# Performance work log

Measured on AMD Instinct MI355X. Metric: run time of the kernel, lower is better.

The kernel has to match this reference:

```python
import jax, jax.numpy as jnp
import numpy as np

H = 1024
B_SZ = 4
L = 2048


def setup_inputs() -> dict:
    key = jax.random.key(0)
    ks = jax.random.split(key, 7)
    s_in = 1.0 / np.sqrt(H)
    x = jax.random.normal(ks[0], (B_SZ, L, H), dtype=jnp.float32)
    # torch nn.Linear weights: (out_features, in_features)
    W_proj = jax.random.uniform(ks[1], (4 * H, H), minval=-s_in, maxval=s_in, dtype=jnp.float32)
    W_delta = jax.random.uniform(ks[2], (H, H), minval=-s_in, maxval=s_in, dtype=jnp.float32)
    b_delta = jax.random.uniform(ks[3], (H,), minval=-s_in, maxval=s_in, dtype=jnp.float32)
    A = 0.02 * jax.random.normal(ks[4], (1, 1, H), dtype=jnp.float32)
    Bp = 0.02 * jax.random.normal(ks[5], (1, H, 1), dtype=jnp.float32)
    D = jnp.ones((1,), dtype=jnp.float32)
    return {"x": x, "W_proj": W_proj, "A": A, "Bp": Bp, "D": D, "W_delta": W_delta, "b_delta": b_delta}


def reference(x, W_proj, A, Bp, D, W_delta, b_delta):
    # x: (b, l, h)
    h = x.shape[-1]
    proj = x @ W_proj.T                                   # (b, l, 4h)
    delta, Bs, Cs, residual = jnp.split(proj, 4, axis=-1) # each (b, l, h)
    delta = jax.nn.softplus(delta @ W_delta.T + b_delta)  # (b, l, h)
    A1 = A[0, 0]       # (h,)
    B1 = Bp[0, :, 0]   # (h,)
    # discretization: dA[b,h,l] = exp(delta*A)[b,l,h] * B1[h] (n-dim of Bp has size 1)
    dA = jnp.exp(delta * A1) * B1                         # (b, l, h), layout transposed vs torch
    # dB[b,h,0,l] = cumsum_l(delta[b,l,h] * B1[h])
    dB = jnp.cumsum(delta * B1, axis=1)                   # (b, l, h)
    # selective_scan: y[b,h,l] = sum_n (dA[b,h,l]*u[b,h,n] + dB[b,h,0,l]) * C[b,h,n]
    # sum over n distributes: y = dA * sum_n(u*C) + dB * sum_n(C)
    uC = jnp.sum(x * Cs, axis=1, keepdims=True)           # (b, 1, h)
    Csum = jnp.sum(Cs, axis=1, keepdims=True)             # (b, 1, h)
    y = dA * uC + dB * Csum                               # (b, l, h)
    return y + residual * D
```

## Files before the change

### kernel.cpp

```cpp
#include <hip/hip_runtime.h>
#include <hip/hip_bf16.h>
#include <cstdint>

#define H 1024
#define BSZ 4
#define LSEQ 2048
#define M_TOT (BSZ*LSEQ)
#define NCH 32
#define LCH (LSEQ/NCH)

typedef __attribute__((ext_vector_type(4))) float  f32x4;
typedef __attribute__((ext_vector_type(2))) float  f32x2;
typedef __attribute__((ext_vector_type(8))) __bf16 bf16x8;
typedef __attribute__((ext_vector_type(4))) __bf16 bf16x4;
typedef __attribute__((ext_vector_type(2))) __bf16 bf16x2;

typedef __attribute__((address_space(1))) unsigned int as1_u32;
typedef __attribute__((address_space(3))) unsigned int as3_u32;

__device__ __forceinline__ void gld_lds16(const void* g, const void* l) {
    as1_u32* gp = reinterpret_cast<as1_u32*>((uintptr_t)g);
    as3_u32* lp = reinterpret_cast<as3_u32*>((uint32_t)(uintptr_t)l);
    __builtin_amdgcn_global_load_lds(gp, lp, 16, 0, 0);
}

__device__ __forceinline__ float softplus_fast(float f) {
    return fmaxf(f, 0.f) + __logf(1.f + __expf(-fabsf(f)));
}

template<int KT, int MODE>
__global__ __launch_bounds__(256, 3) void gemm_bt(
    const __bf16* __restrict__ A,
    const __bf16* __restrict__ B,
    __bf16* __restrict__ O0,
    __bf16* __restrict__ O2,
    const __bf16* __restrict__ xb,
    const float* __restrict__ bias,
    float* __restrict__ pD,
    float* __restrict__ pUp,
    float* __restrict__ pCp)
{
    constexpr int K = KT * 32;
    __shared__ __align__(16) __bf16 lds[17408];

    const int tid  = threadIdx.x;
    const int lane = tid & 63;
    const int wid  = tid >> 6;
    const int wr   = (wid >> 1) * 64;
    const int wc   = (wid & 1) * 64;
    const int l15  = lane & 15;
    const int quad = lane >> 4;

    const int row0 = blockIdx.y * 128;
    const int col0 = blockIdx.x * 128;

    const int srow = lane >> 2;
    const int soct = (lane & 3) ^ ((lane >> 3) & 3);
    const __bf16* ag0 = A + (size_t)(row0 + (wid    )*16 + srow) * K + soct*8;
    const __bf16* ag1 = A + (size_t)(row0 + (wid + 4)*16 + srow) * K + soct*8;
    const __bf16* bg0 = B + (size_t)(col0 + (wid    )*16 + srow) * K + soct*8;
    const __bf16* bg1 = B + (size_t)(col0 + (wid + 4)*16 + srow) * K + soct*8;
    const int lA0 = (wid    )*512;
    const int lA1 = (wid + 4)*512;
    const int lB0 = 4096 + (wid    )*512;
    const int lB1 = 4096 + (wid + 4)*512;

    const int sw = (l15 >> 1) & 3;
    int aoff[4], boff[4];
#pragma unroll
    for (int i = 0; i < 4; ++i) {
        aoff[i] =        ((wr + i*16 + l15) * 4 + (quad ^ sw)) * 8;
        boff[i] = 4096 + ((wc + i*16 + l15) * 4 + (quad ^ sw)) * 8;
    }

    f32x4 acc[4][4] = {};

    auto stage = [&](int buf) {
        __bf16* base = lds + buf * 8192;
        gld_lds16(ag0, base + lA0);
        gld_lds16(ag1, base + lA1);
        gld_lds16(bg0, base + lB0);
        gld_lds16(bg1, base + lB1);
        ag0 += 32; ag1 += 32; bg0 += 32; bg1 += 32;
    };
    auto compute = [&](int buf) {
        const __bf16* base = lds + buf * 8192;
        bf16x8 af[4], bf[4];
#pragma unroll
        for (int i = 0; i < 4; ++i) af[i] = *(const bf16x8*)(base + aoff[i]);
#pragma unroll
        for (int j = 0; j < 4; ++j) bf[j] = *(const bf16x8*)(base + boff[j]);
#pragma unroll
        for (int i = 0; i < 4; ++i)
#pragma unroll
            for (int j = 0; j < 4; ++j)
                acc[i][j] = __builtin_amdgcn_mfma_f32_16x16x32_bf16(
                    af[i], bf[j], acc[i][j], 0, 0, 0);
    };

    stage(0);
#pragma unroll 2
    for (int kt = 0; kt < KT; ++kt) {
        __syncthreads();
        if (kt + 1 < KT) stage((kt + 1) & 1);
        compute(kt & 1);
    }

    const int colb = (col0 & 1023) + wc + l15;
    const int rowb = row0 + wr + quad*4;

    if (MODE == 0) {
#pragma unroll
        for (int i = 0; i < 4; ++i)
#pragma unroll
            for (int j = 0; j < 4; ++j) {
                const int col = colb + j*16;
#pragma unroll
                for (int r = 0; r < 4; ++r)
                    O0[(size_t)(rowb + i*16 + r) * H + col] = (__bf16)acc[i][j][r];
            }
    } else {
        const int seg = col0 >> 10;
        if (seg == 0) {
            const int chunk = (row0 + wr) >> 6;
#pragma unroll
            for (int j = 0; j < 4; ++j) {
                const int col = colb + j*16;
                const float bv = bias[col];
                float s = 0.f;
#pragma unroll
                for (int i = 0; i < 4; ++i)
#pragma unroll
                    for (int r = 0; r < 4; ++r) {
                        float f = softplus_fast(acc[i][j][r] + bv);
                        O0[(size_t)(rowb + i*16 + r) * H + col] = (__bf16)f;
                        s += f;
                    }
                s += __shfl_down(s, 32); s += __shfl_down(s, 16);
                if (quad == 0) pD[chunk*H + col] = s;
            }
        } else if (seg == 1) {
            __syncthreads();
#pragma unroll
            for (int i = 0; i < 4; ++i)
#pragma unroll
                for (int j = 0; j < 4; ++j) {
                    const int lrow0 = wr + quad*4 + i*16;
                    const int lcol  = wc + j*16 + l15;
#pragma unroll
                    for (int r = 0; r < 4; ++r)
                        lds[(lrow0 + r)*136 + lcol] = (__bf16)acc[i][j][r];
                }
            __syncthreads();
            const int g   = tid >> 4;
            const int oct = tid & 15;
            const int gc0 = (col0 & 1023) + oct*8;
            float su[8] = {}, sc[8] = {};
#pragma unroll
            for (int rr = 0; rr < 8; ++rr) {
                const int lrow = g*8 + rr;
                bf16x8 cv = *(const bf16x8*)(lds + lrow*136 + oct*8);
                bf16x8 xv = *(const bf16x8*)(xb + (size_t)(row0 + lrow)*H + gc0);
#pragma unroll
                for (int q = 0; q < 8; ++q) {
                    float c = (float)cv[q];
                    su[q] += (float)xv[q] * c;
                    sc[q] += c;
                }
            }
            float* pf = reinterpret_cast<float*>(lds);
            __syncthreads();
#pragma unroll
            for (int q = 0; q < 8; ++q) {
                pf[g*128 + oct*8 + q]        = su[q];
                pf[2048 + g*128 + oct*8 + q] = sc[q];
            }
            __syncthreads();
            const int col = tid & 127;
            const int rb  = row0 >> 7;
            float s = 0.f;
            if (tid < 128) {
#pragma unroll
                for (int g2 = 0; g2 < 16; ++g2) s += pf[g2*128 + col];
                pUp[rb*H + (col0 & 1023) + col] = s;
            } else {
#pragma unroll
                for (int g2 = 0; g2 < 16; ++g2) s += pf[2048 + g2*128 + col];
                pCp[rb*H + (col0 & 1023) + col] = s;
            }
        } else {
#pragma unroll
            for (int i = 0; i < 4; ++i)
#pragma unroll
                for (int j = 0; j < 4; ++j) {
                    const int col = colb + j*16;
#pragma unroll
                    for (int r = 0; r < 4; ++r)
                        O2[(size_t)(rowb + i*16 + r) * H + col] = (__bf16)acc[i][j][r];
                }
        }
    }
}

#define XB 8192
#define PB 2048
#define DB 1024
#define TB 256
__global__ void cast_kernel(const float* __restrict__ x,
                            const float* __restrict__ Wp,
                            const float* __restrict__ Wd,
                            __bf16* __restrict__ xb,
                            __bf16* __restrict__ Wpb,
                            __bf16* __restrict__ Wdb,
                            __bf16* __restrict__ Wp1T)
{
    __shared__ __bf16 tlds[64*65];
    const int t = threadIdx.x;
    const int bidx = blockIdx.x;

    if (bidx < XB + PB + DB) {
        const f32x4* src; __bf16* dst; int si, di;
        if (bidx < XB) {
            int i = bidx*256 + t;
            src = (const f32x4*)x;  si = i; dst = xb;  di = i;
        } else if (bidx < XB + PB) {
            int j = (bidx - XB)*256 + t;
            int row = j >> 8, cf = j & 255;
            src = (const f32x4*)Wp; si = (2048 + row)*256 + cf;
            dst = Wpb; di = (1024 + row)*256 + cf;
        } else {
            int j = (bidx - XB - PB)*256 + t;
            src = (const f32x4*)Wd; si = j; dst = Wdb; di = j;
        }
        f32x4 v = src[si];
        bf16x4 o = { (__bf16)v[0], (__bf16)v[1], (__bf16)v[2], (__bf16)v[3] };
        *(bf16x4*)(dst + (size_t)di*4) = o;
    } else {
        int tt = bidx - (XB + PB + DB);
        int ty = tt >> 4, tx = tt & 15;
        int rb = t >> 4, cb = t & 15;
#pragma unroll
        for (int rr = 0; rr < 4; ++rr) {
            int row = rb*4 + rr;
            f32x4 v = *(const f32x4*)(Wp + (size_t)(ty*64 + row)*1024 + tx*64 + cb*4);
#pragma unroll
            for (int q = 0; q < 4; ++q)
                tlds[row*65 + cb*4 + q] = (__bf16)v[q];
        }
        __syncthreads();
#pragma unroll
        for (int rr = 0; rr < 4; ++rr) {
            int kk = rb*4 + rr;
            bf16x4 o = { tlds[(cb*4+0)*65 + kk], tlds[(cb*4+1)*65 + kk],
                         tlds[(cb*4+2)*65 + kk], tlds[(cb*4+3)*65 + kk] };
            *(bf16x4*)(Wp1T + (size_t)(tx*64 + kk)*1024 + ty*64 + cb*4) = o;
        }
    }
}

__global__ void final_kernel(const __bf16* __restrict__ delta,
                             const __bf16* __restrict__ res,
                             const float* __restrict__ pD,
                             const float* __restrict__ pUp,
                             const float* __restrict__ pCp,
                             const float* __restrict__ Av,
                             const float* __restrict__ Bv,
                             const float* __restrict__ Dv,
                             float* __restrict__ out)
{
    const int c = blockIdx.x, b = blockIdx.z;
    const int h0 = blockIdx.y * 512 + threadIdx.x * 2;
    float run0 = 0.f, run1 = 0.f;
    for (int cp = 0; cp < c; ++cp) {
        f32x2 v = *(const f32x2*)(pD + (b*NCH + cp)*H + h0);
        run0 += v[0]; run1 += v[1];
    }
    float uc0 = 0.f, uc1 = 0.f, cs0 = 0.f, cs1 = 0.f;
#pragma unroll
    for (int i = 0; i < 16; ++i) {
        f32x2 u = *(const f32x2*)(pUp + (b*16 + i)*H + h0);
        f32x2 s = *(const f32x2*)(pCp + (b*16 + i)*H + h0);
        uc0 += u[0]; uc1 += u[1]; cs0 += s[0]; cs1 += s[1];
    }
    const f32x2 a1 = *(const f32x2*)(Av + h0);
    const f32x2 b1 = *(const f32x2*)(Bv + h0);
    const float dd = Dv[0];
    size_t base = ((size_t)(b*LSEQ + c*LCH)) * H + h0;
    for (int l = 0; l < LCH; ++l) {
        size_t idx = base + (size_t)l * H;
        bf16x2 dv2 = *(const bf16x2*)(delta + idx);
        bf16x2 rs2 = *(const bf16x2*)(res + idx);
        float d0 = (float)dv2[0], d1v = (float)dv2[1];
        run0 += d0; run1 += d1v;
        f32x2 o;
        o[0] = __expf(d0*a1[0])*b1[0]*uc0 + run0*b1[0]*cs0 + (float)rs2[0]*dd;
        o[1] = __expf(d1v*a1[1])*b1[1]*uc1 + run1*b1[1]*cs1 + (float)rs2[1]*dd;
        *(f32x2*)(out + idx) = o;
    }
}

extern "C" void kernel_launch(void* const* d_in, const int* in_sizes, int n_in,
                              void* d_out, int out_size, void* d_ws, size_t ws_size,
                              hipStream_t stream)
{
    (void)in_sizes; (void)n_in; (void)out_size; (void)ws_size;
    const float* x  = (const float*)d_in[0];
    const float* Wp = (const float*)d_in[1];
    const float* Av = (const float*)d_in[2];
    const float* Bv = (const float*)d_in[3];
    const float* Dv = (const float*)d_in[4];
    const float* Wd = (const float*)d_in[5];
    const float* bd = (const float*)d_in[6];
    float* out = (float*)d_out;

    char* ws = (char*)d_ws;
    size_t o = 0;
    auto alloc = [&](size_t bytes) {
        void* p = ws + o; o += (bytes + 255) & ~(size_t)255; return p;
    };
    __bf16* xb   = (__bf16*)alloc((size_t)M_TOT * H * 2);
    __bf16* Wpb  = (__bf16*)alloc((size_t)3072 * H * 2);
    __bf16* Wdb  = (__bf16*)alloc((size_t)H * H * 2);
    __bf16* Wp1T = (__bf16*)alloc((size_t)H * H * 2);
    __bf16* resb = (__bf16*)alloc((size_t)M_TOT * H * 2);
    __bf16* db   = (__bf16*)alloc((size_t)M_TOT * H * 2);
    float*  pD   = (float*)alloc((size_t)BSZ * NCH * H * 4);
    float*  pUp  = (float*)alloc((size_t)64 * H * 4);
    float*  pCp  = (float*)alloc((size_t)64 * H * 4);

    cast_kernel<<<XB + PB + DB + TB, 256, 0, stream>>>(
        x, Wp, Wd, xb, Wpb, Wdb, Wp1T);
    gemm_bt<32, 0><<<dim3(8, 8), 256, 0, stream>>>(
        Wdb, Wp1T, Wpb, nullptr, nullptr, nullptr, nullptr, nullptr, nullptr);
    gemm_bt<32, 2><<<dim3(24, 64), 256, 0, stream>>>(
        xb, Wpb, db, resb, xb, bd, pD, pUp, pCp);
    final_kernel<<<dim3(NCH, 2, BSZ), 256, 0, stream>>>(db, resb, pD, pUp, pCp,
                                                        Av, Bv, Dv, out);
}
```

Measured before the change: 203.8 us.

## Fuse cast, weight-fusion GEMM, main GEMM and scan into one persistent kernel

Replaces the four separate launches with a single persistent kernel of 512 blocks that uses global atomic grid barriers between phases. The W_delta·W_proj fusion GEMM now reads fp32 weights directly and casts and transposes them in-register, which removes the separate Wdb/Wp1T cast and transpose pass. The main GEMM tiles are distributed over the persistent blocks, and the scan chunk count doubles to 64 so all 512 blocks have work in the final phase. This removes launch gaps and intermediate buffers, at the cost of spin barriers, a reliance on all 512 blocks being co-resident, and a slower, uncoalesced LDS staging path for the weight GEMM.

```diff
diff --git a/kernel.cpp b/kernel.cpp
--- a/kernel.cpp
+++ b/kernel.cpp
@@ -6,8 +6,9 @@
 #define BSZ 4
 #define LSEQ 2048
 #define M_TOT (BSZ*LSEQ)
-#define NCH 32
+#define NCH 64
 #define LCH (LSEQ/NCH)
+#define NBLK 512
 
 typedef __attribute__((ext_vector_type(4))) float  f32x4;
 typedef __attribute__((ext_vector_type(2))) float  f32x2;
@@ -28,88 +29,114 @@
     return fmaxf(f, 0.f) + __logf(1.f + __expf(-fabsf(f)));
 }
 
-template<int KT, int MODE>
-__global__ __launch_bounds__(256, 3) void gemm_bt(
-    const __bf16* __restrict__ A,
-    const __bf16* __restrict__ B,
-    __bf16* __restrict__ O0,
-    __bf16* __restrict__ O2,
-    const __bf16* __restrict__ xb,
-    const float* __restrict__ bias,
-    float* __restrict__ pD,
-    float* __restrict__ pUp,
-    float* __restrict__ pCp)
+__device__ __forceinline__ void grid_bar(unsigned* cnt, unsigned target) {
+    __syncthreads();
+    if (threadIdx.x == 0) {
+        __hip_atomic_fetch_add(cnt, 1u, __ATOMIC_RELEASE,
+                               __HIP_MEMORY_SCOPE_AGENT);
+        while (__hip_atomic_load(cnt, __ATOMIC_RELAXED,
+                                 __HIP_MEMORY_SCOPE_AGENT) < target)
+            __builtin_amdgcn_s_sleep(2);
+    }
+    __syncthreads();
+    __builtin_amdgcn_fence(__ATOMIC_ACQUIRE, "agent");
+}
+
+__device__ __forceinline__ void mfma_tile(const __bf16* base, const int* aoff,
+                                          const int* boff, f32x4 (&acc)[4][4]) {
+    bf16x8 af[4], bf[4];
+#pragma unroll
+    for (int i = 0; i < 4; ++i) af[i] = *(const bf16x8*)(base + aoff[i]);
+#pragma unroll
+    for (int j = 0; j < 4; ++j) bf[j] = *(const bf16x8*)(base + boff[j]);
+#pragma unroll
+    for (int i = 0; i < 4; ++i)
+#pragma unroll
+        for (int j = 0; j < 4; ++j)
+            acc[i][j] = __builtin_amdgcn_mfma_f32_16x16x32_bf16(
+                af[i], bf[j], acc[i][j], 0, 0, 0);
+}
+
+__device__ __forceinline__ void stage_wfuse(__bf16* base,
+        const float* __restrict__ Wd, const float* __restrict__ Wp,
+        int row0f, int col0f, int kt, int tid) {
+    {
+        const int arow = tid & 127, ahalf = tid >> 7;
+        const float* ap = Wd + (size_t)(row0f + arow)*1024 + kt*32 + ahalf*16;
+        f32x4 v0 = *(const f32x4*)(ap);
+        f32x4 v1 = *(const f32x4*)(ap + 4);
+        f32x4 v2 = *(const f32x4*)(ap + 8);
+        f32x4 v3 = *(const f32x4*)(ap + 12);
+        bf16x8 g0 = {(__bf16)v0[0],(__bf16)v0[1],(__bf16)v0[2],(__bf16)v0[3],
+                     (__bf16)v1[0],(__bf16)v1[1],(__bf16)v1[2],(__bf16)v1[3]};
+        bf16x8 g1 = {(__bf16)v2[0],(__bf16)v2[1],(__bf16)v2[2],(__bf16)v2[3],
+                     (__bf16)v3[0],(__bf16)v3[1],(__bf16)v3[2],(__bf16)v3[3]};
+        const int swz = (arow >> 1) & 3;
+        *(bf16x8*)(base + (arow*4 + ((ahalf*2    ) ^ swz))*8) = g0;
+        *(bf16x8*)(base + (arow*4 + ((ahalf*2 + 1) ^ swz))*8) = g1;
+    }
+    {
+        const int bk = tid >> 3, bgrp = tid & 7;
+        const float* bp = Wp + (size_t)(kt*32 + bk)*1024 + col0f + bgrp*16;
+        float wv[16];
+#pragma unroll
+        for (int q = 0; q < 4; ++q) {
+            f32x4 w = *(const f32x4*)(bp + q*4);
+            wv[q*4+0]=w[0]; wv[q*4+1]=w[1]; wv[q*4+2]=w[2]; wv[q*4+3]=w[3];
+        }
+        const int ko = bk >> 3, ke = bk & 7;
+#pragma unroll
+        for (int q = 0; q < 16; ++q) {
+            const int hp = bgrp*16 + q;
+            base[4096 + (hp*4 + (ko ^ ((hp>>1)&3)))*8 + ke] = (__bf16)wv[q];
+        }
+    }
+}
+
+__global__ __launch_bounds__(256, 3) void fused(
+    const float* __restrict__ x,  const float* __restrict__ Wp,
+    const float* __restrict__ Av, const float* __restrict__ Bv,
+    const float* __restrict__ Dv, const float* __restrict__ Wd,
+    const float* __restrict__ bd,
+    __bf16* __restrict__ xb,   __bf16* __restrict__ Wpb,
+    __bf16* __restrict__ resb, __bf16* __restrict__ db,
+    float* __restrict__ pD, float* __restrict__ pUp, float* __restrict__ pCp,
+    unsigned* __restrict__ cnt, float* __restrict__ out)
 {
-    constexpr int K = KT * 32;
     __shared__ __align__(16) __bf16 lds[17408];
 
     const int tid  = threadIdx.x;
+    const int bid  = blockIdx.x;
     const int lane = tid & 63;
     const int wid  = tid >> 6;
     const int wr   = (wid >> 1) * 64;
     const int wc   = (wid & 1) * 64;
     const int l15  = lane & 15;
     const int quad = lane >> 4;
-
-    const int row0 = blockIdx.y * 128;
-    const int col0 = blockIdx.x * 128;
-
-    const int srow = lane >> 2;
-    const int soct = (lane & 3) ^ ((lane >> 3) & 3);
-    const __bf16* ag0 = A + (size_t)(row0 + (wid    )*16 + srow) * K + soct*8;
-    const __bf16* ag1 = A + (size_t)(row0 + (wid + 4)*16 + srow) * K + soct*8;
-    const __bf16* bg0 = B + (size_t)(col0 + (wid    )*16 + srow) * K + soct*8;
-    const __bf16* bg1 = B + (size_t)(col0 + (wid + 4)*16 + srow) * K + soct*8;
-    const int lA0 = (wid    )*512;
-    const int lA1 = (wid + 4)*512;
-    const int lB0 = 4096 + (wid    )*512;
-    const int lB1 = 4096 + (wid + 4)*512;
-
-    const int sw = (l15 >> 1) & 3;
+    const int sw   = (l15 >> 1) & 3;
     int aoff[4], boff[4];
 #pragma unroll
     for (int i = 0; i < 4; ++i) {
         aoff[i] =        ((wr + i*16 + l15) * 4 + (quad ^ sw)) * 8;
         boff[i] = 4096 + ((wc + i*16 + l15) * 4 + (quad ^ sw)) * 8;
     }
-
-    f32x4 acc[4][4] = {};
-
-    auto stage = [&](int buf) {
-        __bf16* base = lds + buf * 8192;
-        gld_lds16(ag0, base + lA0);
-        gld_lds16(ag1, base + lA1);
-        gld_lds16(bg0, base + lB0);
-        gld_lds16(bg1, base + lB1);
-        ag0 += 32; ag1 += 32; bg0 += 32; bg1 += 32;
-    };
-    auto compute = [&](int buf) {
-        const __bf16* base = lds + buf * 8192;
-        bf16x8 af[4], bf[4];
-#pragma unroll
-        for (int i = 0; i < 4; ++i) af[i] = *(const bf16x8*)(base + aoff[i]);
-#pragma unroll
-        for (int j = 0; j < 4; ++j) bf[j] = *(const bf16x8*)(base + boff[j]);
-#pragma unroll
-        for (int i = 0; i < 4; ++i)
-#pragma unroll
-            for (int j = 0; j < 4; ++j)
-                acc[i][j] = __builtin_amdgcn_mfma_f32_16x16x32_bf16(
-                    af[i], bf[j], acc[i][j], 0, 0, 0);
-    };
-
-    stage(0);
+    const int srow = lane >> 2;
+    const int soct = (lane & 3) ^ ((lane >> 3) & 3);
+
+    if (bid < 64) {
+        const int row0f = (bid >> 3) * 128;
+        const int col0f = (bid & 7) * 128;
+        f32x4 acc[4][4] = {};
+        stage_wfuse(lds, Wd, Wp, row0f, col0f, 0, tid);
 #pragma unroll 2
-    for (int kt = 0; kt < KT; ++kt) {
-        __syncthreads();
-        if (kt + 1 < KT) stage((kt + 1) & 1);
-        compute(kt & 1);
-    }
-
-    const int colb = (col0 & 1023) + wc + l15;
-    const int rowb = row0 + wr + quad*4;
-
-    if (MODE == 0) {
+        for (int kt = 0; kt < 32; ++kt) {
+            __syncthreads();
+            if (kt + 1 < 32)
+                stage_wfuse(lds + ((kt+1)&1)*8192, Wd, Wp, row0f, col0f, kt+1, tid);
+            mfma_tile(lds + (kt&1)*8192, aoff, boff, acc);
+        }
+        const int colb = col0f + wc + l15;
+        const int rowb = row0f + wr + quad*4;
 #pragma unroll
         for (int i = 0; i < 4; ++i)
 #pragma unroll
@@ -117,27 +144,87 @@
                 const int col = colb + j*16;
 #pragma unroll
                 for (int r = 0; r < 4; ++r)
-                    O0[(size_t)(rowb + i*16 + r) * H + col] = (__bf16)acc[i][j][r];
+                    Wpb[(size_t)(rowb + i*16 + r) * H + col] = (__bf16)acc[i][j][r];
             }
     } else {
-        const int seg = col0 >> 10;
+        for (int task = bid - 64; task < 10240; task += 448) {
+            const f32x4* src; __bf16* dst; int si, di;
+            if (task < 8192) {
+                int i = task*256 + tid;
+                src = (const f32x4*)x;  si = i; dst = xb;  di = i;
+            } else {
+                int j = (task - 8192)*256 + tid;
+                int row = j >> 8, cf = j & 255;
+                src = (const f32x4*)Wp; si = (2048 + row)*256 + cf;
+                dst = Wpb; di = (1024 + row)*256 + cf;
+            }
+            f32x4 v = src[si];
+            bf16x4 o = { (__bf16)v[0], (__bf16)v[1], (__bf16)v[2], (__bf16)v[3] };
+            *(bf16x4*)(dst + (size_t)di*4) = o;
+        }
+    }
+
+    grid_bar(cnt, NBLK);
+
+    for (int task = bid; task < 1536; task += NBLK) {
+        const int cx = task / 64;
+        const int ry = task % 64;
+        const int row0 = ry * 128;
+        const int col0 = cx * 128;
+        __syncthreads();
+
+        const __bf16* ag0 = xb  + (size_t)(row0 + (wid    )*16 + srow)*H + soct*8;
+        const __bf16* ag1 = xb  + (size_t)(row0 + (wid + 4)*16 + srow)*H + soct*8;
+        const __bf16* bg0 = Wpb + (size_t)(col0 + (wid    )*16 + srow)*H + soct*8;
+        const __bf16* bg1 = Wpb + (size_t)(col0 + (wid + 4)*16 + srow)*H + soct*8;
+        const int lA0 = (wid    )*512, lA1 = (wid + 4)*512;
+        const int lB0 = 4096 + (wid    )*512, lB1 = 4096 + (wid + 4)*512;
+
+        f32x4 acc[4][4] = {};
+        {
+            gld_lds16(ag0, lds + lA0); gld_lds16(ag1, lds + lA1);
+            gld_lds16(bg0, lds + lB0); gld_lds16(bg1, lds + lB1);
+            ag0 += 32; ag1 += 32; bg0 += 32; bg1 += 32;
+        }
+#pragma unroll 2
+        for (int kt = 0; kt < 32; ++kt) {
+            __syncthreads();
+            if (kt + 1 < 32) {
+                __bf16* base = lds + ((kt+1)&1)*8192;
+                gld_lds16(ag0, base + lA0); gld_lds16(ag1, base + lA1);
+                gld_lds16(bg0, base + lB0); gld_lds16(bg1, base + lB1);
+                ag0 += 32; ag1 += 32; bg0 += 32; bg1 += 32;
+            }
+            mfma_tile(lds + (kt&1)*8192, aoff, boff, acc);
+        }
+
+        const int colb = (col0 & 1023) + wc + l15;
+        const int rowb = row0 + wr + quad*4;
+        const int seg  = col0 >> 10;
         if (seg == 0) {
-            const int chunk = (row0 + wr) >> 6;
+            const int c0 = (row0 + wr) >> 5;
 #pragma unroll
             for (int j = 0; j < 4; ++j) {
                 const int col = colb + j*16;
-                const float bv = bias[col];
-                float s = 0.f;
-#pragma unroll
-                for (int i = 0; i < 4; ++i)
+                const float bv = bd[col];
+                float slo = 0.f, shi = 0.f;
+#pragma unroll
+                for (int i = 0; i < 4; ++i) {
+                    float part = 0.f;
 #pragma unroll
                     for (int r = 0; r < 4; ++r) {
                         float f = softplus_fast(acc[i][j][r] + bv);
-                        O0[(size_t)(rowb + i*16 + r) * H + col] = (__bf16)f;
-                        s += f;
+                        db[(size_t)(rowb + i*16 + r) * H + col] = (__bf16)f;
+                        part += f;
                     }
-                s += __shfl_down(s, 32); s += __shfl_down(s, 16);
-                if (quad == 0) pD[chunk*H + col] = s;
+                    if (i < 2) slo += part; else shi += part;
+                }
+                slo += __shfl_down(slo, 32); slo += __shfl_down(slo, 16);
+                shi += __shfl_down(shi, 32); shi += __shfl_down(shi, 16);
+                if (quad == 0) {
+                    pD[c0*H + col]     = slo;
+                    pD[(c0+1)*H + col] = shi;
+                }
             }
         } else if (seg == 1) {
             __syncthreads();
@@ -196,106 +283,46 @@
                     const int col = colb + j*16;
 #pragma unroll
                     for (int r = 0; r < 4; ++r)
-                        O2[(size_t)(rowb + i*16 + r) * H + col] = (__bf16)acc[i][j][r];
-                }
-        }
-    }
-}
-
-#define XB 8192
-#define PB 2048
-#define DB 1024
-#define TB 256
-__global__ void cast_kernel(const float* __restrict__ x,
-                            const float* __restrict__ Wp,
-                            const float* __restrict__ Wd,
-                            __bf16* __restrict__ xb,
-                            __bf16* __restrict__ Wpb,
-                            __bf16* __restrict__ Wdb,
-                            __bf16* __restrict__ Wp1T)
-{
-    __shared__ __bf16 tlds[64*65];
-    const int t = threadIdx.x;
-    const int bidx = blockIdx.x;
-
-    if (bidx < XB + PB + DB) {
-        const f32x4* src; __bf16* dst; int si, di;
-        if (bidx < XB) {
-            int i = bidx*256 + t;
-            src = (const f32x4*)x;  si = i; dst = xb;  di = i;
-        } else if (bidx < XB + PB) {
-            int j = (bidx - XB)*256 + t;
-            int row = j >> 8, cf = j & 255;
-            src = (const f32x4*)Wp; si = (2048 + row)*256 + cf;
-            dst = Wpb; di = (1024 + row)*256 + cf;
-        } else {
-            int j = (bidx - XB - PB)*256 + t;
-            src = (const f32x4*)Wd; si = j; dst = Wdb; di = j;
-        }
-        f32x4 v = src[si];
-        bf16x4 o = { (__bf16)v[0], (__bf16)v[1], (__bf16)v[2], (__bf16)v[3] };
-        *(bf16x4*)(dst + (size_t)di*4) = o;
-    } else {
-        int tt = bidx - (XB + PB + DB);
-        int ty = tt >> 4, tx = tt & 15;
-        int rb = t >> 4, cb = t & 15;
-#pragma unroll
-        for (int rr = 0; rr < 4; ++rr) {
-            int row = rb*4 + rr;
-            f32x4 v = *(const f32x4*)(Wp + (size_t)(ty*64 + row)*1024 + tx*64 + cb*4);
-#pragma unroll
-            for (int q = 0; q < 4; ++q)
-                tlds[row*65 + cb*4 + q] = (__bf16)v[q];
-        }
-        __syncthreads();
-#pragma unroll
-        for (int rr = 0; rr < 4; ++rr) {
-            int kk = rb*4 + rr;
-            bf16x4 o = { tlds[(cb*4+0)*65 + kk], tlds[(cb*4+1)*65 + kk],
-                         tlds[(cb*4+2)*65 + kk], tlds[(cb*4+3)*65 + kk] };
-            *(bf16x4*)(Wp1T + (size_t)(tx*64 + kk)*1024 + ty*64 + cb*4) = o;
-        }
-    }
-}
-
-__global__ void final_kernel(const __bf16* __restrict__ delta,
-                             const __bf16* __restrict__ res,
-                             const float* __restrict__ pD,
-                             const float* __restrict__ pUp,
-                             const float* __restrict__ pCp,
-                             const float* __restrict__ Av,
-                             const float* __restrict__ Bv,
-                             const float* __restrict__ Dv,
-                             float* __restrict__ out)
-{
-    const int c = blockIdx.x, b = blockIdx.z;
-    const int h0 = blockIdx.y * 512 + threadIdx.x * 2;
-    float run0 = 0.f, run1 = 0.f;
-    for (int cp = 0; cp < c; ++cp) {
-        f32x2 v = *(const f32x2*)(pD + (b*NCH + cp)*H + h0);
-        run0 += v[0]; run1 += v[1];
-    }
-    float uc0 = 0.f, uc1 = 0.f, cs0 = 0.f, cs1 = 0.f;
-#pragma unroll
-    for (int i = 0; i < 16; ++i) {
-        f32x2 u = *(const f32x2*)(pUp + (b*16 + i)*H + h0);
-        f32x2 s = *(const f32x2*)(pCp + (b*16 + i)*H + h0);
-        uc0 += u[0]; uc1 += u[1]; cs0 += s[0]; cs1 += s[1];
-    }
-    const f32x2 a1 = *(const f32x2*)(Av + h0);
-    const f32x2 b1 = *(const f32x2*)(Bv + h0);
-    const float dd = Dv[0];
-    size_t base = ((size_t)(b*LSEQ + c*LCH)) * H + h0;
-    for (int l = 0; l < LCH; ++l) {
-        size_t idx = base + (size_t)l * H;
-        bf16x2 dv2 = *(const bf16x2*)(delta + idx);
-        bf16x2 rs2 = *(const bf16x2*)(res + idx);
-        float d0 = (float)dv2[0], d1v = (float)dv2[1];
-        run0 += d0; run1 += d1v;
-        f32x2 o;
-        o[0] = __expf(d0*a1[0])*b1[0]*uc0 + run0*b1[0]*cs0 + (float)rs2[0]*dd;
-        o[1] = __expf(d1v*a1[1])*b1[1]*uc1 + run1*b1[1]*cs1 + (float)rs2[1]*dd;
-        *(f32x2*)(out + idx) = o;
+                        resb[(size_t)(rowb + i*16 + r) * H + col] = (__bf16)acc[i][j][r];
+                }
+        }
+    }
+
+    grid_bar(cnt, 2u * NBLK);
+
+    {
+        const int b = bid >> 7;
+        const int rest = bid & 127;
+        const int c = rest >> 1;
+        const int y = rest & 1;
+        const int h0 = y*512 + tid*2;
+        float run0 = 0.f, run1 = 0.f;
+        for (int cp = 0; cp < c; ++cp) {
+            f32x2 v = *(const f32x2*)(pD + (b*NCH + cp)*H + h0);
+            run0 += v[0]; run1 += v[1];
+        }
+        float uc0 = 0.f, uc1 = 0.f, cs0 = 0.f, cs1 = 0.f;
+#pragma unroll
+        for (int i = 0; i < 16; ++i) {
+            f32x2 u = *(const f32x2*)(pUp + (b*16 + i)*H + h0);
+            f32x2 s = *(const f32x2*)(pCp + (b*16 + i)*H + h0);
+            uc0 += u[0]; uc1 += u[1]; cs0 += s[0]; cs1 += s[1];
+        }
+        const f32x2 a1 = *(const f32x2*)(Av + h0);
+        const f32x2 b1 = *(const f32x2*)(Bv + h0);
+        const float dd = Dv[0];
+        size_t base = ((size_t)(b*LSEQ + c*LCH)) * H + h0;
+        for (int l = 0; l < LCH; ++l) {
+            size_t idx = base + (size_t)l * H;
+            bf16x2 dv2 = *(const bf16x2*)(db + idx);
+            bf16x2 rs2 = *(const bf16x2*)(resb + idx);
+            float d0 = (float)dv2[0], d1v = (float)dv2[1];
+            run0 += d0; run1 += d1v;
+            f32x2 o;
+            o[0] = __expf(d0*a1[0])*b1[0]*uc0 + run0*b1[0]*cs0 + (float)rs2[0]*dd;
+            o[1] = __expf(d1v*a1[1])*b1[1]*uc1 + run1*b1[1]*cs1 + (float)rs2[1]*dd;
+            *(f32x2*)(out + idx) = o;
+        }
     }
 }
 
@@ -320,20 +347,15 @@
     };
     __bf16* xb   = (__bf16*)alloc((size_t)M_TOT * H * 2);
     __bf16* Wpb  = (__bf16*)alloc((size_t)3072 * H * 2);
-    __bf16* Wdb  = (__bf16*)alloc((size_t)H * H * 2);
-    __bf16* Wp1T = (__bf16*)alloc((size_t)H * H * 2);
     __bf16* resb = (__bf16*)alloc((size_t)M_TOT * H * 2);
     __bf16* db   = (__bf16*)alloc((size_t)M_TOT * H * 2);
     float*  pD   = (float*)alloc((size_t)BSZ * NCH * H * 4);
     float*  pUp  = (float*)alloc((size_t)64 * H * 4);
     float*  pCp  = (float*)alloc((size_t)64 * H * 4);
-
-    cast_kernel<<<XB + PB + DB + TB, 256, 0, stream>>>(
-        x, Wp, Wd, xb, Wpb, Wdb, Wp1T);
-    gemm_bt<32, 0><<<dim3(8, 8), 256, 0, stream>>>(
-        Wdb, Wp1T, Wpb, nullptr, nullptr, nullptr, nullptr, nullptr, nullptr);
-    gemm_bt<32, 2><<<dim3(24, 64), 256, 0, stream>>>(
-        xb, Wpb, db, resb, xb, bd, pD, pUp, pCp);
-    final_kernel<<<dim3(NCH, 2, BSZ), 256, 0, stream>>>(db, resb, pD, pUp, pCp,
-                                                        Av, Bv, Dv, out);
-}
+    unsigned* cnt = (unsigned*)alloc(256);
+
+    (void)hipMemsetAsync(cnt, 0, 256, stream);
+    fused<<<NBLK, 256, 0, stream>>>(x, Wp, Av, Bv, Dv, Wd, bd,
+                                    xb, Wpb, resb, db, pD, pUp, pCp, cnt,
+                                    out);
+}
```

Result: slower. 358.3 us (+75.9%).
